# Optimization experiments

Hardware: AMD Instinct MI355X
Metric: run time of the kernel (lower is better)

Reference implementation:

```python
import jax, jax.numpy as jnp
import numpy as np

NUM_Q = 8      # num_quantizers
K = 1024       # codebook_size (num_tokens)
D = 512        # feature dim
B, T = 16, 2000
BETA = 0.25    # commitment weight


def setup_inputs() -> dict:
    key = jax.random.key(0)
    kx, kc = jax.random.split(key)
    x = jax.random.normal(kx, (B, T, D), dtype=jnp.float32)
    # learned codebooks, one per quantizer stage: [NUM_Q, K, D]
    codebooks = jax.random.normal(kc, (NUM_Q, K, D), dtype=jnp.float32)
    return {"x": x, "codebooks": codebooks}


def _vq_stage(residual, codebook):
    """Single VQ layer: nearest-codeword search + straight-through + commitment loss.
    residual: [B, T, D]; codebook: [K, D]."""
    sg = jax.lax.stop_gradient
    # squared L2 distances via ||r||^2 - 2 r.e + ||e||^2  -> [B, T, K]
    r2 = jnp.sum(residual * residual, axis=-1, keepdims=True)          # [B,T,1]
    e2 = jnp.sum(codebook * codebook, axis=-1)                          # [K]
    dots = jnp.einsum('btd,kd->btk', residual, codebook)                # [B,T,K]
    dist = r2 - 2.0 * dots + e2
    indices = jnp.argmin(dist, axis=-1)                                 # [B,T] int
    quantized = codebook[indices]                                       # [B,T,D] gather
    # commitment + codebook loss (VQ-VAE style)
    loss = (BETA * jnp.mean((sg(quantized) - residual) ** 2)
            + jnp.mean((quantized - sg(residual)) ** 2))
    # straight-through estimator
    quantized_st = residual + sg(quantized - residual)
    return quantized_st, indices, loss


def reference(x, codebooks):
    def step(carry, codebook):
        residual, q_out = carry
        q, idx, loss = _vq_stage(residual, codebook)
        residual = residual - jax.lax.stop_gradient(q)
        return (residual, q_out + q), (idx, loss)

    init = (x, jnp.zeros_like(x))
    (_, quantized_out), (all_indices, all_losses) = jax.lax.scan(step, init, codebooks)
    # all_indices: [NUM_Q, B, T]; mean loss across stages
    return quantized_out, all_indices, jnp.mean(all_losses)
```

## Files before the change

### kernel.cpp

```cpp
#include <hip/hip_runtime.h>

#define M_TOK 32000
#define DIM   512
#define KCB   1024
#define NQ    8
#define BM 64
#define BN 256
#define BK 32
#define KSTEPS (DIM / BK)

typedef _Float16 f16x8 __attribute__((ext_vector_type(8)));
typedef _Float16 f16x4 __attribute__((ext_vector_type(4)));
typedef float f32x4 __attribute__((ext_vector_type(4)));

__device__ __forceinline__ float wave_reduce_sum(float v) {
#pragma unroll
  for (int off = 32; off > 0; off >>= 1) v += __shfl_xor(v, off, 64);
  return v;
}

__device__ __forceinline__ unsigned int fenc(float f) {
  unsigned int u = __float_as_uint(f);
  return (u & 0x80000000u) ? ~u : (u | 0x80000000u);
}

__device__ __forceinline__ int swz(int row, int k) {
  return (row * 64 + k * 2) ^ ((row & 7) << 4);
}

__global__ __launch_bounds__(256) void rvq_init_kernel(
    const float* __restrict__ x, const float* __restrict__ cb,
    float* __restrict__ e2, float* __restrict__ r2,
    unsigned long long* __restrict__ keys, float* __restrict__ lossCell) {
  if (blockIdx.x == 0 && threadIdx.x == 0) *lossCell = 0.f;
  for (int i = blockIdx.x * 256 + threadIdx.x; i < M_TOK; i += gridDim.x * 256)
    keys[i] = ~0ull;
  int row = blockIdx.x * 4 + (threadIdx.x >> 6);
  int lane = threadIdx.x & 63;
  const float* src;
  float* dst;
  if (row < NQ * KCB) {
    src = cb + (size_t)row * DIM;
    dst = e2 + row;
  } else {
    int t = row - NQ * KCB;
    if (t >= M_TOK) return;
    src = x + (size_t)t * DIM;
    dst = r2 + t;
  }
  const float4* s4 = (const float4*)src;
  float s = 0.f;
  float4 v = s4[lane];
  s += v.x * v.x + v.y * v.y + v.z * v.z + v.w * v.w;
  v = s4[lane + 64];
  s += v.x * v.x + v.y * v.y + v.z * v.z + v.w * v.w;
  s = wave_reduce_sum(s);
  if (lane == 0) *dst = s;
}

__global__ __launch_bounds__(256) void rvq_split_cb_kernel(
    const float* __restrict__ cb, _Float16* __restrict__ cbh,
    _Float16* __restrict__ cbl) {
  size_t i4 = (size_t)blockIdx.x * 256 + threadIdx.x;
  if (i4 >= (size_t)NQ * KCB * DIM / 4) return;
  float4 v = ((const float4*)cb)[i4];
  f16x4 h, l;
  float vv[4] = {v.x, v.y, v.z, v.w};
#pragma unroll
  for (int j = 0; j < 4; ++j) {
    _Float16 hh = (_Float16)vv[j];
    h[j] = hh;
    l[j] = (_Float16)(vv[j] - (float)hh);
  }
  ((f16x4*)cbh)[i4] = h;
  ((f16x4*)cbl)[i4] = l;
}

__global__ __launch_bounds__(256, 3) void rvq_argmin_kernel(
    const float* __restrict__ rin,
    const _Float16* __restrict__ cbh,
    const _Float16* __restrict__ cbl,
    const float* __restrict__ e2,
    const float* __restrict__ r2in,
    unsigned long long* __restrict__ keys) {
  const int bid = blockIdx.x;
  const int m = (bid >> 5) * 8 + (bid & 7);
  if (m >= M_TOK / BM) return;
  const int ncl = (bid >> 3) & 3;
  const int m0 = m * BM;
  const int n0 = ncl * BN;

  __shared__ __align__(16) _Float16 sAhi[BM * BK];
  __shared__ __align__(16) _Float16 sAlo[BM * BK];
  __shared__ __align__(16) _Float16 sBhi[BN * BK];
  __shared__ __align__(16) _Float16 sBlo[BN * BK];
  __shared__ float e2s[BN];
  __shared__ float r2s[BM];

  const int tid = threadIdx.x;
  const int lane = tid & 63, wn = tid >> 6;
  const int l15 = lane & 15, l4 = lane >> 4;

  e2s[tid] = e2[n0 + tid];
  if (tid < BM) r2s[tid] = r2in[m0 + tid];

  f32x4 acc[4][4];
#pragma unroll
  for (int a = 0; a < 4; ++a)
#pragma unroll
    for (int b = 0; b < 4; ++b) acc[a][b] = (f32x4){0.f, 0.f, 0.f, 0.f};

  for (int ks = 0; ks < KSTEPS; ++ks) {
    const int kc = ks * BK;
    __syncthreads();
#pragma unroll
    for (int t = 0; t < 2; ++t) {
      int p = tid + t * 256;
      int row = p >> 3, kk = (p & 7) * 4;
      float4 v = *(const float4*)(rin + (size_t)(m0 + row) * DIM + kc + kk);
      float vv[4] = {v.x, v.y, v.z, v.w};
      f16x4 h, l;
#pragma unroll
      for (int j = 0; j < 4; ++j) {
        _Float16 hh = (_Float16)vv[j];
        h[j] = hh;
        l[j] = (_Float16)(vv[j] - (float)hh);
      }
      int off = swz(row, kk);
      *(f16x4*)((char*)sAhi + off) = h;
      *(f16x4*)((char*)sAlo + off) = l;
    }
#pragma unroll
    for (int it = 0; it < 4; ++it) {
      int c = tid + it * 256;
      int r = c >> 2, slot = c & 3;
      size_t gsrc = (size_t)(n0 + r) * DIM + kc + slot * 8;
      int off = swz(r, slot * 8);
      *(uint4*)((char*)sBhi + off) = *(const uint4*)(cbh + gsrc);
      *(uint4*)((char*)sBlo + off) = *(const uint4*)(cbl + gsrc);
    }
    __syncthreads();
    f16x8 ah[4], al[4];
#pragma unroll
    for (int mf = 0; mf < 4; ++mf) {
      int off = swz(mf * 16 + l15, l4 * 8);
      ah[mf] = *(const f16x8*)((const char*)sAhi + off);
      al[mf] = *(const f16x8*)((const char*)sAlo + off);
    }
#pragma unroll
    for (int nf = 0; nf < 4; ++nf) {
      int off = swz(wn * 64 + nf * 16 + l15, l4 * 8);
      f16x8 bh = *(const f16x8*)((const char*)sBhi + off);
      f16x8 bl = *(const f16x8*)((const char*)sBlo + off);
#pragma unroll
      for (int mf = 0; mf < 4; ++mf) {
        acc[mf][nf] = __builtin_amdgcn_mfma_f32_16x16x32_f16(ah[mf], bh, acc[mf][nf], 0, 0, 0);
        acc[mf][nf] = __builtin_amdgcn_mfma_f32_16x16x32_f16(ah[mf], bl, acc[mf][nf], 0, 0, 0);
        acc[mf][nf] = __builtin_amdgcn_mfma_f32_16x16x32_f16(al[mf], bh, acc[mf][nf], 0, 0, 0);
      }
    }
  }

  float minv[16];
  int mini[16];
#pragma unroll
  for (int i = 0; i < 16; ++i) { minv[i] = 3.4e38f; mini[i] = 0; }
#pragma unroll
  for (int nf = 0; nf < 4; ++nf) {
    int col_l = wn * 64 + nf * 16 + l15;
    float e2v = e2s[col_l];
    int colg = n0 + col_l;
#pragma unroll
    for (int mf = 0; mf < 4; ++mf) {
#pragma unroll
      for (int rr = 0; rr < 4; ++rr) {
        float d = (r2s[mf * 16 + l4 * 4 + rr] - 2.f * acc[mf][nf][rr]) + e2v;
        int i = mf * 4 + rr;
        if (d < minv[i]) { minv[i] = d; mini[i] = colg; }
      }
    }
  }
#pragma unroll
  for (int mf = 0; mf < 4; ++mf) {
#pragma unroll
    for (int rr = 0; rr < 4; ++rr) {
      int i = mf * 4 + rr;
      float v = minv[i];
      int ix = mini[i];
#pragma unroll
      for (int off = 8; off; off >>= 1) {
        float ov = __shfl_xor(v, off, 16);
        int oi = __shfl_xor(ix, off, 16);
        if (ov < v || (ov == v && oi < ix)) { v = ov; ix = oi; }
      }
      if (l15 == 0) {
        int tok = m0 + mf * 16 + l4 * 4 + rr;
        unsigned long long key = ((unsigned long long)fenc(v) << 32) | (unsigned)ix;
        atomicMin(&keys[tok], key);
      }
    }
  }
}

__global__ __launch_bounds__(256) void rvq_update_kernel(
    const float* __restrict__ rin, const float* __restrict__ cb,
    unsigned long long* __restrict__ keys,
    float* __restrict__ rout, float* __restrict__ r2out,
    float* __restrict__ idx_out, float* __restrict__ lossCell) {
  const int wave = threadIdx.x >> 6, lane = threadIdx.x & 63;
  __shared__ float lred[4];
  float lpart = 0.f;
  for (int r = wave; r < 64; r += 4) {
    const int tok = blockIdx.x * 64 + r;
    const unsigned idx = (unsigned)(keys[tok] & 0xffffffffu);
    const float4* rrow = (const float4*)(rin + (size_t)tok * DIM);
    const float4* crow = (const float4*)(cb + (size_t)idx * DIM);
    float4* orow = (float4*)(rout + (size_t)tok * DIM);
    float ssq_t = 0.f, ssq_r = 0.f;
#pragma unroll
    for (int c4 = 0; c4 < 2; ++c4) {
      int c = lane + c4 * 64;
      float4 a = rrow[c], q = crow[c];
      float4 t = make_float4(q.x - a.x, q.y - a.y, q.z - a.z, q.w - a.w);
      float4 qst = make_float4(a.x + t.x, a.y + t.y, a.z + t.z, a.w + t.w);
      float4 rn = make_float4(a.x - qst.x, a.y - qst.y, a.z - qst.z, a.w - qst.w);
      orow[c] = rn;
      ssq_t += t.x * t.x + t.y * t.y + t.z * t.z + t.w * t.w;
      ssq_r += rn.x * rn.x + rn.y * rn.y + rn.z * rn.z + rn.w * rn.w;
    }
    float tot_t = wave_reduce_sum(ssq_t);
    float tot_r = wave_reduce_sum(ssq_r);
    if (lane == 0) {
      idx_out[tok] = (float)idx;
      keys[tok] = ~0ull;
      r2out[tok] = tot_r;
      lpart += tot_t;
    }
  }
  if (lane == 0) lred[wave] = lpart;
  __syncthreads();
  if (threadIdx.x == 0)
    atomicAdd(lossCell, lred[0] + lred[1] + lred[2] + lred[3]);
}

__global__ __launch_bounds__(256) void rvq_finalize_kernel(
    const float* __restrict__ x, float* __restrict__ out,
    const float* __restrict__ lossCell, float* __restrict__ loss_out) {
  size_t i = (size_t)blockIdx.x * 256 + threadIdx.x;
  const size_t n4 = (size_t)M_TOK * DIM / 4;
  if (i < n4) {
    const float4* x4 = (const float4*)x;
    float4* o4 = (float4*)out;
    float4 a = x4[i], r = o4[i];
    o4[i] = make_float4(a.x - r.x, a.y - r.y, a.z - r.z, a.w - r.w);
  }
  if (blockIdx.x == 0 && threadIdx.x == 0) {
    *loss_out = *lossCell * (1.25f / 131072000.f);
  }
}

extern "C" void kernel_launch(void* const* d_in, const int* in_sizes, int n_in,
                              void* d_out, int out_size, void* d_ws, size_t ws_size,
                              hipStream_t stream) {
  const float* x = (const float*)d_in[0];
  const float* cb = (const float*)d_in[1];
  float* out = (float*)d_out;
  float* idx_out = out + (size_t)M_TOK * DIM;
  float* loss_out = idx_out + (size_t)NQ * M_TOK;

  char* w = (char*)d_ws;
  unsigned long long* keys = (unsigned long long*)w;
  float* e2 = (float*)(w + 256000);
  float* r2 = (float*)(w + 289792);
  float* lossCell = (float*)(w + 417792);
  _Float16* cbh = (_Float16*)(w + 417808 + 240);
  _Float16* cbl = cbh + (size_t)NQ * KCB * DIM;

  {
    int rows = NQ * KCB + M_TOK;
    rvq_init_kernel<<<(rows + 3) / 4, 256, 0, stream>>>(x, cb, e2, r2, keys, lossCell);
    int n4 = NQ * KCB * DIM / 4;
    rvq_split_cb_kernel<<<n4 / 256, 256, 0, stream>>>(cb, cbh, cbl);
  }
  float* resbuf = out;
  const int nsuper = ((M_TOK / BM) + 7) / 8;
  for (int s = 0; s < NQ; ++s) {
    const float* rin = (s == 0) ? x : resbuf;
    const float* cbs = cb + (size_t)s * KCB * DIM;
    rvq_argmin_kernel<<<nsuper * 32, 256, 0, stream>>>(
        rin, cbh + (size_t)s * KCB * DIM, cbl + (size_t)s * KCB * DIM,
        e2 + s * KCB, r2, keys);
    rvq_update_kernel<<<M_TOK / 64, 256, 0, stream>>>(
        rin, cbs, keys, resbuf, r2, idx_out + (size_t)s * M_TOK, lossCell);
  }
  rvq_finalize_kernel<<<(M_TOK * DIM / 4 + 255) / 256, 256, 0, stream>>>(
      x, out, lossCell, loss_out);
}
```

Measured before the change: 1.213 ms.

## Pre-swizzle codebook into MFMA fragment layout and double-buffer via direct global-to-LDS loads

The codebook hi/lo split is now stored in a fragment-major layout matching the MFMA operand order, so B tiles are copied straight into LDS with global_load_lds and read back without swizzle math. The argmin main loop is double-buffered: the next k-step's A and B loads are issued before the current MFMAs, with manual waitcnt, a single barrier per step and raised wave priority during compute. The block-to-tile mapping and occupancy bound (3 to 2) also change. The aim is to hide global-load latency and cut LDS address overhead, at the cost of more LDS per block and fragile hand-written wait counts.

```diff
diff --git a/kernel.cpp b/kernel.cpp
--- a/kernel.cpp
+++ b/kernel.cpp
@@ -6,13 +6,22 @@
 #define NQ    8
 #define BM 64
 #define BN 256
-#define BK 32
-#define KSTEPS (DIM / BK)
+#define KS 16
 
 typedef _Float16 f16x8 __attribute__((ext_vector_type(8)));
 typedef _Float16 f16x4 __attribute__((ext_vector_type(4)));
 typedef float f32x4 __attribute__((ext_vector_type(4)));
 
+#define FENCE() __builtin_amdgcn_sched_barrier(0)
+#define WAIT_VM(N) asm volatile("s_waitcnt vmcnt(" #N ")" ::: "memory")
+#define WAIT_LGKM0() asm volatile("s_waitcnt lgkmcnt(0)" ::: "memory")
+
+__device__ __forceinline__ void gload_lds16(const void* g, void* l) {
+  __builtin_amdgcn_global_load_lds(
+      (const __attribute__((address_space(1))) unsigned int*)g,
+      (__attribute__((address_space(3))) unsigned int*)l, 16, 0, 0);
+}
+
 __device__ __forceinline__ float wave_reduce_sum(float v) {
 #pragma unroll
   for (int off = 32; off > 0; off >>= 1) v += __shfl_xor(v, off, 64);
@@ -22,10 +31,6 @@
 __device__ __forceinline__ unsigned int fenc(float f) {
   unsigned int u = __float_as_uint(f);
   return (u & 0x80000000u) ? ~u : (u | 0x80000000u);
-}
-
-__device__ __forceinline__ int swz(int row, int k) {
-  return (row * 64 + k * 2) ^ ((row & 7) << 4);
 }
 
 __global__ __launch_bounds__(256) void rvq_init_kernel(
@@ -59,50 +64,52 @@
 }
 
 __global__ __launch_bounds__(256) void rvq_split_cb_kernel(
-    const float* __restrict__ cb, _Float16* __restrict__ cbh,
-    _Float16* __restrict__ cbl) {
-  size_t i4 = (size_t)blockIdx.x * 256 + threadIdx.x;
-  if (i4 >= (size_t)NQ * KCB * DIM / 4) return;
-  float4 v = ((const float4*)cb)[i4];
-  f16x4 h, l;
-  float vv[4] = {v.x, v.y, v.z, v.w};
-#pragma unroll
-  for (int j = 0; j < 4; ++j) {
-    _Float16 hh = (_Float16)vv[j];
+    const float* __restrict__ cb, _Float16* __restrict__ cbF) {
+  int gid = blockIdx.x * 256 + threadIdx.x;
+  if (gid >= NQ * 16 * 4 * 4 * 4 * 64) return;
+  int lane = gid & 63;
+  int nf = (gid >> 6) & 3;
+  int w  = (gid >> 8) & 3;
+  int nc = (gid >> 10) & 3;
+  int ks = (gid >> 12) & 15;
+  int s  = gid >> 16;
+  int col = nc * 256 + w * 64 + nf * 16 + (lane & 15);
+  int kbase = ks * 32 + (lane >> 4) * 8;
+  const float* src = cb + ((size_t)s * KCB + col) * DIM + kbase;
+  f16x8 h, l;
+#pragma unroll
+  for (int j = 0; j < 8; ++j) {
+    float v = src[j];
+    _Float16 hh = (_Float16)v;
     h[j] = hh;
-    l[j] = (_Float16)(vv[j] - (float)hh);
-  }
-  ((f16x4*)cbh)[i4] = h;
-  ((f16x4*)cbl)[i4] = l;
-}
-
-__global__ __launch_bounds__(256, 3) void rvq_argmin_kernel(
+    l[j] = (_Float16)(v - (float)hh);
+  }
+  size_t base = ((((size_t)((s * 16 + ks) * 4 + nc) * 4 + w) * 8 + nf * 2) * 64
+                 + lane) * 8;
+  *(f16x8*)(cbF + base) = h;
+  *(f16x8*)(cbF + base + 512) = l;
+}
+
+__global__ __launch_bounds__(256, 2) void rvq_argmin_kernel(
     const float* __restrict__ rin,
-    const _Float16* __restrict__ cbh,
-    const _Float16* __restrict__ cbl,
+    const _Float16* __restrict__ cbF,
     const float* __restrict__ e2,
-    const float* __restrict__ r2in,
+    const float* __restrict__ r2,
     unsigned long long* __restrict__ keys) {
-  const int bid = blockIdx.x;
-  const int m = (bid >> 5) * 8 + (bid & 7);
-  if (m >= M_TOK / BM) return;
-  const int ncl = (bid >> 3) & 3;
+  __shared__ __align__(16) _Float16 bufB[2][4][8][512];
+  __shared__ __align__(16) _Float16 bufA[2][4][2][512];
+
+  const int tid = threadIdx.x;
+  const int lane = tid & 63, w = tid >> 6;
+  const int l15 = lane & 15, l4 = lane >> 4;
+  const int x = blockIdx.x & 7, i = blockIdx.x >> 3;
+  const int nc = x >> 1;
+  const int m = (x & 1) * 250 + i;
   const int m0 = m * BM;
-  const int n0 = ncl * BN;
-
-  __shared__ __align__(16) _Float16 sAhi[BM * BK];
-  __shared__ __align__(16) _Float16 sAlo[BM * BK];
-  __shared__ __align__(16) _Float16 sBhi[BN * BK];
-  __shared__ __align__(16) _Float16 sBlo[BN * BK];
-  __shared__ float e2s[BN];
-  __shared__ float r2s[BM];
-
-  const int tid = threadIdx.x;
-  const int lane = tid & 63, wn = tid >> 6;
-  const int l15 = lane & 15, l4 = lane >> 4;
-
-  e2s[tid] = e2[n0 + tid];
-  if (tid < BM) r2s[tid] = r2in[m0 + tid];
+  const int c0 = nc * BN;
+
+  const _Float16* gB = cbF + (((size_t)nc * 4 + w) * 8) * 512 + (size_t)lane * 8;
+  const int p0 = tid, p1 = tid + 256;
 
   f32x4 acc[4][4];
 #pragma unroll
@@ -110,48 +117,65 @@
 #pragma unroll
     for (int b = 0; b < 4; ++b) acc[a][b] = (f32x4){0.f, 0.f, 0.f, 0.f};
 
-  for (int ks = 0; ks < KSTEPS; ++ks) {
-    const int kc = ks * BK;
-    __syncthreads();
-#pragma unroll
-    for (int t = 0; t < 2; ++t) {
-      int p = tid + t * 256;
-      int row = p >> 3, kk = (p & 7) * 4;
-      float4 v = *(const float4*)(rin + (size_t)(m0 + row) * DIM + kc + kk);
-      float vv[4] = {v.x, v.y, v.z, v.w};
-      f16x4 h, l;
-#pragma unroll
-      for (int j = 0; j < 4; ++j) {
-        _Float16 hh = (_Float16)vv[j];
-        h[j] = hh;
-        l[j] = (_Float16)(vv[j] - (float)hh);
-      }
-      int off = swz(row, kk);
-      *(f16x4*)((char*)sAhi + off) = h;
-      *(f16x4*)((char*)sAlo + off) = l;
-    }
-#pragma unroll
-    for (int it = 0; it < 4; ++it) {
-      int c = tid + it * 256;
-      int r = c >> 2, slot = c & 3;
-      size_t gsrc = (size_t)(n0 + r) * DIM + kc + slot * 8;
-      int off = swz(r, slot * 8);
-      *(uint4*)((char*)sBhi + off) = *(const uint4*)(cbh + gsrc);
-      *(uint4*)((char*)sBlo + off) = *(const uint4*)(cbl + gsrc);
-    }
-    __syncthreads();
+  float4 a0, a1;
+  auto ldA = [&](int ks, int p) {
+    return *(const float4*)(rin + (size_t)(m0 + (p >> 3)) * DIM + ks * 32 + (p & 7) * 4);
+  };
+  auto cvtWriteA = [&](int buf, const float4& v, int p) {
+    int r = p >> 3, kg = p & 7;
+    int mf = r >> 4, lp = (kg >> 1) * 16 + (r & 15), fo = (kg & 1) * 4;
+    float vv[4] = {v.x, v.y, v.z, v.w};
+    f16x4 h, l;
+#pragma unroll
+    for (int j = 0; j < 4; ++j) {
+      _Float16 hh = (_Float16)vv[j];
+      h[j] = hh;
+      l[j] = (_Float16)(vv[j] - (float)hh);
+    }
+    *(f16x4*)&bufA[buf][mf][0][lp * 8 + fo] = h;
+    *(f16x4*)&bufA[buf][mf][1][lp * 8 + fo] = l;
+  };
+  a0 = ldA(0, p0);
+  a1 = ldA(0, p1);
+  FENCE();
+#pragma unroll
+  for (int c = 0; c < 8; ++c)
+    gload_lds16(gB + c * 512, &bufB[0][w][c][0]);
+  WAIT_VM(8);
+  FENCE();
+  cvtWriteA(0, a0, p0);
+  cvtWriteA(0, a1, p1);
+
+  for (int ks = 0; ks < KS; ++ks) {
+    const int cur = ks & 1;
+    if (ks < KS - 1) {
+      a0 = ldA(ks + 1, p0);
+      a1 = ldA(ks + 1, p1);
+      FENCE();
+      const _Float16* gBs = gB + (size_t)(ks + 1) * 65536;
+#pragma unroll
+      for (int c = 0; c < 8; ++c)
+        gload_lds16(gBs + c * 512, &bufB[cur ^ 1][w][c][0]);
+      WAIT_VM(10);
+    } else {
+      WAIT_VM(0);
+    }
+    FENCE();
+    WAIT_LGKM0();
+    FENCE();
+    __builtin_amdgcn_s_barrier();
+    FENCE();
     f16x8 ah[4], al[4];
 #pragma unroll
     for (int mf = 0; mf < 4; ++mf) {
-      int off = swz(mf * 16 + l15, l4 * 8);
-      ah[mf] = *(const f16x8*)((const char*)sAhi + off);
-      al[mf] = *(const f16x8*)((const char*)sAlo + off);
-    }
+      ah[mf] = *(const f16x8*)&bufA[cur][mf][0][lane * 8];
+      al[mf] = *(const f16x8*)&bufA[cur][mf][1][lane * 8];
+    }
+    __builtin_amdgcn_s_setprio(1);
 #pragma unroll
     for (int nf = 0; nf < 4; ++nf) {
-      int off = swz(wn * 64 + nf * 16 + l15, l4 * 8);
-      f16x8 bh = *(const f16x8*)((const char*)sBhi + off);
-      f16x8 bl = *(const f16x8*)((const char*)sBlo + off);
+      f16x8 bh = *(const f16x8*)&bufB[cur][w][nf * 2][lane * 8];
+      f16x8 bl = *(const f16x8*)&bufB[cur][w][nf * 2 + 1][lane * 8];
 #pragma unroll
       for (int mf = 0; mf < 4; ++mf) {
         acc[mf][nf] = __builtin_amdgcn_mfma_f32_16x16x32_f16(ah[mf], bh, acc[mf][nf], 0, 0, 0);
@@ -159,24 +183,34 @@
         acc[mf][nf] = __builtin_amdgcn_mfma_f32_16x16x32_f16(al[mf], bh, acc[mf][nf], 0, 0, 0);
       }
     }
-  }
-
+    __builtin_amdgcn_s_setprio(0);
+    if (ks < KS - 1) {
+      cvtWriteA(cur ^ 1, a0, p0);
+      cvtWriteA(cur ^ 1, a1, p1);
+    }
+  }
+
+  float rv[4][4];
+#pragma unroll
+  for (int mf = 0; mf < 4; ++mf) {
+    float4 q = *(const float4*)(r2 + m0 + mf * 16 + l4 * 4);
+    rv[mf][0] = q.x; rv[mf][1] = q.y; rv[mf][2] = q.z; rv[mf][3] = q.w;
+  }
   float minv[16];
   int mini[16];
 #pragma unroll
-  for (int i = 0; i < 16; ++i) { minv[i] = 3.4e38f; mini[i] = 0; }
+  for (int i2 = 0; i2 < 16; ++i2) { minv[i2] = 3.4e38f; mini[i2] = 0; }
 #pragma unroll
   for (int nf = 0; nf < 4; ++nf) {
-    int col_l = wn * 64 + nf * 16 + l15;
-    float e2v = e2s[col_l];
-    int colg = n0 + col_l;
+    int col = c0 + w * 64 + nf * 16 + l15;
+    float e2v = e2[col];
 #pragma unroll
     for (int mf = 0; mf < 4; ++mf) {
 #pragma unroll
       for (int rr = 0; rr < 4; ++rr) {
-        float d = (r2s[mf * 16 + l4 * 4 + rr] - 2.f * acc[mf][nf][rr]) + e2v;
-        int i = mf * 4 + rr;
-        if (d < minv[i]) { minv[i] = d; mini[i] = colg; }
+        float d = (rv[mf][rr] - 2.f * acc[mf][nf][rr]) + e2v;
+        int ii = mf * 4 + rr;
+        if (d < minv[ii]) { minv[ii] = d; mini[ii] = col; }
       }
     }
   }
@@ -184,9 +218,9 @@
   for (int mf = 0; mf < 4; ++mf) {
 #pragma unroll
     for (int rr = 0; rr < 4; ++rr) {
-      int i = mf * 4 + rr;
-      float v = minv[i];
-      int ix = mini[i];
+      int ii = mf * 4 + rr;
+      float v = minv[ii];
+      int ix = mini[ii];
 #pragma unroll
       for (int off = 8; off; off >>= 1) {
         float ov = __shfl_xor(v, off, 16);
@@ -268,30 +302,27 @@
   float* idx_out = out + (size_t)M_TOK * DIM;
   float* loss_out = idx_out + (size_t)NQ * M_TOK;
 
-  char* w = (char*)d_ws;
-  unsigned long long* keys = (unsigned long long*)w;
-  float* e2 = (float*)(w + 256000);
-  float* r2 = (float*)(w + 289792);
-  float* lossCell = (float*)(w + 417792);
-  _Float16* cbh = (_Float16*)(w + 417808 + 240);
-  _Float16* cbl = cbh + (size_t)NQ * KCB * DIM;
+  char* wsp = (char*)d_ws;
+  unsigned long long* keys = (unsigned long long*)wsp;
+  float* e2 = (float*)(wsp + 256000);
+  float* r2 = (float*)(wsp + 288768);
+  float* lossCell = (float*)(wsp + 416768);
+  _Float16* cbF = (_Float16*)(wsp + 416800 + 224);
 
   {
     int rows = NQ * KCB + M_TOK;
     rvq_init_kernel<<<(rows + 3) / 4, 256, 0, stream>>>(x, cb, e2, r2, keys, lossCell);
-    int n4 = NQ * KCB * DIM / 4;
-    rvq_split_cb_kernel<<<n4 / 256, 256, 0, stream>>>(cb, cbh, cbl);
+    rvq_split_cb_kernel<<<NQ * 16 * 4 * 4 * 4 * 64 / 256, 256, 0, stream>>>(cb, cbF);
   }
   float* resbuf = out;
-  const int nsuper = ((M_TOK / BM) + 7) / 8;
+  const size_t stageF = (size_t)16 * 4 * 4 * 8 * 512;
   for (int s = 0; s < NQ; ++s) {
     const float* rin = (s == 0) ? x : resbuf;
-    const float* cbs = cb + (size_t)s * KCB * DIM;
-    rvq_argmin_kernel<<<nsuper * 32, 256, 0, stream>>>(
-        rin, cbh + (size_t)s * KCB * DIM, cbl + (size_t)s * KCB * DIM,
-        e2 + s * KCB, r2, keys);
+    rvq_argmin_kernel<<<(M_TOK / BM) * 4, 256, 0, stream>>>(
+        rin, cbF + (size_t)s * stageF, e2 + s * KCB, r2, keys);
     rvq_update_kernel<<<M_TOK / 64, 256, 0, stream>>>(
-        rin, cbs, keys, resbuf, r2, idx_out + (size_t)s * M_TOK, lossCell);
+        rin, cb + (size_t)s * KCB * DIM, keys, resbuf, r2,
+        idx_out + (size_t)s * M_TOK, lossCell);
   }
   rvq_finalize_kernel<<<(M_TOK * DIM / 4 + 255) / 256, 256, 0, stream>>>(
       x, out, lossCell, loss_out);
```

Result: slower. 1.284 ms (+5.8%).
